# Performance work log

Measured on AMD Instinct MI355X. Metric: run time of the kernel, lower is better.

Reference implementation:

```python
import jax, jax.numpy as jnp
import numpy as np

H = 48; W = 48; C_IN = 32; C_OUT = 64
L = 4                      # liftsamples
RADIUS = 3                 # neighborhood radius
CMCO = 16                  # LieConv PointConv fixed mid channels
FOCAL = W / np.pi          # equidistant fisheye focal
CX, CY = (W - 1) / 2.0, (H - 1) / 2.0
EPS = 1e-7


def _build_neighbor_indices(h, w, radius):
    offs = [(dx, dy) for dy in range(-radius, radius + 1)
            for dx in range(-radius, radius + 1)
            if dx * dx + dy * dy <= radius * radius]
    offs = np.array(offs, dtype=np.int64)  # (k,2) as (dx,dy)
    yy, xx = np.meshgrid(np.arange(h), np.arange(w), indexing='ij')
    yy = yy.reshape(-1, 1); xx = xx.reshape(-1, 1)
    ny = yy + offs[None, :, 1]; nx = xx + offs[None, :, 0]
    valid = (ny >= 0) & (ny < h) & (nx >= 0) & (nx < w)
    idx = ny * w + nx
    return np.where(valid, idx, -1).astype(np.int32)  # (h*w, k)


def swish(x):
    return x * jax.nn.sigmoid(x)


def so3_exp(wvec):
    # Rodrigues: (...,3) -> (...,3,3)
    th = jnp.maximum(jnp.linalg.norm(wvec, axis=-1, keepdims=True), EPS)
    k = wvec / th
    kx, ky, kz = k[..., 0], k[..., 1], k[..., 2]
    z = jnp.zeros_like(kx)
    K = jnp.stack([jnp.stack([z, -kz, ky], -1),
                   jnp.stack([kz, z, -kx], -1),
                   jnp.stack([-ky, kx, z], -1)], -2)
    th = th[..., None]
    I = jnp.eye(3, dtype=wvec.dtype)
    return I + jnp.sin(th) * K + (1.0 - jnp.cos(th)) * (K @ K)


def so3_log(R):
    # (...,3,3) -> (...,3)
    tr = R[..., 0, 0] + R[..., 1, 1] + R[..., 2, 2]
    cos = jnp.clip((tr - 1.0) * 0.5, -1.0 + 1e-6, 1.0 - 1e-6)
    th = jnp.arccos(cos)
    v = jnp.stack([R[..., 2, 1] - R[..., 1, 2],
                   R[..., 0, 2] - R[..., 2, 0],
                   R[..., 1, 0] - R[..., 0, 1]], -1)
    return v * (th / (2.0 * jnp.sin(th)))[..., None]


def setup_inputs() -> dict:
    key = jax.random.key(0)
    ks = jax.random.split(key, 6)
    def lin(k, fi, fo):
        return jax.random.normal(k, (fi, fo), jnp.float32) / np.sqrt(fi)
    return {
        'x': jax.random.normal(ks[0], (2, C_IN, H, W), jnp.float32),
        'neighbor_idx': jnp.asarray(_build_neighbor_indices(H, W, RADIUS)),
        'W1': lin(ks[1], 3, 32), 'b1': jnp.zeros((32,), jnp.float32),
        'W2': lin(ks[2], 32, 32), 'b2': jnp.zeros((32,), jnp.float32),
        'W3': lin(ks[3], 32, CMCO), 'b3': jnp.zeros((CMCO,), jnp.float32),
        'Wl': lin(ks[4], CMCO * C_IN, C_OUT), 'bl': jnp.zeros((C_OUT,), jnp.float32),
    }


def _lift_log(dtype):
    # pixel grid -> unit rays -> so(3) log of lifted group elems, shape (n*L, 3)
    u = jnp.arange(W, dtype=dtype); v = jnp.arange(H, dtype=dtype)
    uu, vv = jnp.meshgrid(u, v)               # 'xy' indexing, (H,W)
    dx = (uu - CX).reshape(-1); dy = (vv - CY).reshape(-1)
    r = jnp.sqrt(dx * dx + dy * dy)
    theta = r / FOCAL
    rs = jnp.maximum(r, EPS)
    rays = jnp.stack([jnp.sin(theta) * dx / rs,
                      jnp.sin(theta) * dy / rs,
                      jnp.cos(theta)], -1)    # (n,3)
    pz = jnp.clip(rays[:, 2], -1.0 + 1e-6, 1.0 - 1e-6)
    ang = jnp.arccos(pz)
    axis = jnp.stack([-rays[:, 1], rays[:, 0], jnp.zeros_like(pz)], -1)
    axis = axis / jnp.maximum(jnp.linalg.norm(axis, axis=-1, keepdims=True), EPS)
    Rp = so3_exp(axis * ang[:, None])          # (n,3,3), Rp @ e3 = ray
    alphas = jnp.arange(L, dtype=dtype) * (2.0 * np.pi / L)
    Rz = so3_exp(jnp.stack([jnp.zeros_like(alphas), jnp.zeros_like(alphas), alphas], -1))
    Rlift = jnp.einsum('nij,ljk->nlik', Rp, Rz)  # (n,L,3,3)
    return so3_log(Rlift).reshape(H * W * L, 3)


def reference(x, neighbor_idx, W1, b1, W2, b2, W3, b3, Wl, bl):
    bs, c, h, w = x.shape
    n = h * w
    k = neighbor_idx.shape[1]
    nL, K = n * L, k * L

    a = _lift_log(x.dtype)                                   # (nL,3)

    valid = neighbor_idx >= 0                                # (n,k)
    safe_pix = jnp.maximum(neighbor_idx, 0).astype(jnp.int32)
    # lifted neighbor indices: query lift copy l sees all (j, l') neighbors
    nb_lift = safe_pix[:, None, :, None] * L + jnp.arange(L, dtype=jnp.int32)[None, None, None, :]
    nb_lift = jnp.broadcast_to(nb_lift, (n, L, k, L)).reshape(nL, K)
    nb_pix = jnp.broadcast_to(safe_pix[:, None, :, None], (n, L, k, L)).reshape(nL, K)
    mask = jnp.broadcast_to(valid[:, None, :, None], (n, L, k, L)).reshape(nL, K)

    # pairwise group elements: log(exp(-b) @ exp(a))
    b_log = a[nb_lift]                                       # (nL,K,3)
    Rab = jnp.einsum('qmij,qjk->qmik', so3_exp(-b_log), so3_exp(a))
    ab = so3_log(Rab)                                        # (nL,K,3)

    # kernel MLP (WeightNet: 3 -> 32 -> 32 -> 16, swish)
    hdn = swish(ab @ W1 + b1)
    hdn = swish(hdn @ W2 + b2)
    wts = swish(hdn @ W3 + b3)                               # (nL,K,16)
    wts = jnp.where(mask[..., None], wts, 0.0)

    values = x.transpose(0, 2, 3, 1).reshape(bs, n, c)       # (bs,n,c)
    nv = values[:, nb_pix]                                   # (bs,nL,K,c)
    partial = jnp.einsum('bqmc,qmf->bqcf', nv, wts).reshape(bs, nL, c * CMCO)
    out = partial @ Wl + bl                                  # (bs,nL,c_out)
    out = out.reshape(bs, n, L, -1).mean(axis=2)             # pool over lift samples
    return out.reshape(bs, h, w, -1).transpose(0, 3, 1, 2)   # (bs,c_out,h,w)
```

## Files before the change

kernel.cpp:

```cpp
#include <hip/hip_runtime.h>

#define WW   48
#define NPIX 2304
#define CIN  32
#define COUT 64
#define KNB  29
#define FCO  16
#define NPJ  (NPIX * KNB)

#define WS_RP64 0
#define WS_EG   165888
#define WS_M0   1050624
#define WS_V    1050688
#define WS_PART 4257856

__device__ __forceinline__ float swish_f(float x) {
    return x * __builtin_amdgcn_rcpf(1.0f + __expf(-x));
}

__device__ __forceinline__ void so3_exp_d(double wx, double wy, double wz, double R[9]) {
    double n  = sqrt(wx * wx + wy * wy + wz * wz);
    double th = fmax(n, 1e-7);
    double kx = wx / th, ky = wy / th, kz = wz / th;
    double s = sin(th), c = cos(th);
    double omc = 1.0 - c;
    R[0] = 1.0 + omc * (kx * kx - 1.0);
    R[1] = -s * kz + omc * kx * ky;
    R[2] =  s * ky + omc * kx * kz;
    R[3] =  s * kz + omc * kx * ky;
    R[4] = 1.0 + omc * (ky * ky - 1.0);
    R[5] = -s * kx + omc * ky * kz;
    R[6] = -s * ky + omc * kz * kx;
    R[7] =  s * kx + omc * kz * ky;
    R[8] = 1.0 + omc * (kz * kz - 1.0);
}

__device__ __forceinline__ void compute_Rp_d(int p, double R[9]) {
    int ui = p % WW, vi = p / WW;
    double dx = (double)ui - 23.5;
    double dy = (double)vi - 23.5;
    double r  = sqrt(dx * dx + dy * dy);
    const double FOCAL = 48.0 / 3.14159265358979323846;
    double theta = r / FOCAL;
    double rs = fmax(r, 1e-7);
    double st = sin(theta);
    double rayx = st * dx / rs;
    double rayy = st * dy / rs;
    double rayz = cos(theta);
    double pz  = fmin(fmax(rayz, -1.0 + 1e-6), 1.0 - 1e-6);
    double ang = acos(pz);
    double ax = -rayy, ay = rayx;
    double an = fmax(sqrt(ax * ax + ay * ay), 1e-7);
    ax /= an; ay /= an;
    so3_exp_d(ax * ang, ay * ang, 0.0, R);
}

__device__ __forceinline__ void mlp_half(float ab0, float ab1, float ab2, int Q0,
    const float* __restrict__ W1, const float* __restrict__ b1,
    const float* __restrict__ W2, const float* __restrict__ b2,
    const float* __restrict__ W3, const float* __restrict__ b3,
    float* acc3) {
    float accq[16];
    #pragma unroll
    for (int q = 0; q < 16; ++q) accq[q] = b2[Q0 + q];
    #pragma unroll
    for (int i = 0; i < 32; ++i) {
        float h = swish_f(b1[i] + ab0 * W1[i] + ab1 * W1[32 + i] + ab2 * W1[64 + i]);
        #pragma unroll
        for (int q = 0; q < 16; ++q) accq[q] += h * W2[i * 32 + Q0 + q];
    }
    #pragma unroll
    for (int q = 0; q < 16; ++q) {
        float h2 = swish_f(accq[q]);
        #pragma unroll
        for (int f = 0; f < FCO; ++f) acc3[f] += h2 * W3[(Q0 + q) * FCO + f];
    }
}

__device__ __forceinline__ void mlp_eval(float ab0, float ab1, float ab2,
    const float* __restrict__ W1, const float* __restrict__ b1,
    const float* __restrict__ W2, const float* __restrict__ b2,
    const float* __restrict__ W3, const float* __restrict__ b3,
    float* o) {
    float acc3[FCO];
    #pragma unroll
    for (int f = 0; f < FCO; ++f) acc3[f] = b3[f];
    mlp_half(ab0, ab1, ab2, 0,  W1, b1, W2, b2, W3, b3, acc3);
    __builtin_amdgcn_sched_barrier(0);
    mlp_half(ab0, ab1, ab2, 16, W1, b1, W2, b2, W3, b3, acc3);
    #pragma unroll
    for (int f = 0; f < FCO; ++f) o[f] = swish_f(acc3[f]);
}

__global__ __launch_bounds__(256)
void prep_kernel(const float* __restrict__ W1, const float* __restrict__ b1,
                 const float* __restrict__ W2, const float* __restrict__ b2,
                 const float* __restrict__ W3, const float* __restrict__ b3,
                 double* __restrict__ rp64, float* __restrict__ eg,
                 float* __restrict__ m0v) {
    int g = blockIdx.x * 256 + threadIdx.x;
    if (g > NPIX * 6) return;
    if (g == NPIX * 6) {
        float o[FCO];
        mlp_eval(0.f, 0.f, 0.f, W1, b1, W2, b2, W3, b3, o);
        #pragma unroll
        for (int f = 0; f < FCO; ++f) m0v[f] = o[f];
        return;
    }
    int pix = g / 6, which = g - pix * 6;
    double R[9];
    compute_Rp_d(pix, R);
    if (which == 0) {
        #pragma unroll
        for (int e = 0; e < 9; ++e) rp64[pix * 9 + e] = R[e];
    }
    int m = (which < 3) ? which : (which - 3);
    int l = m + (m >> 1);
    double c = (l == 0) ? 1.0 : 0.0;
    double s = (l == 1) ? 1.0 : ((l == 3) ? -1.0 : 0.0);
    double M[9];
    #pragma unroll
    for (int i = 0; i < 3; ++i) {
        M[i * 3 + 0] =  R[i * 3 + 0] * c + R[i * 3 + 1] * s;
        M[i * 3 + 1] = -R[i * 3 + 0] * s + R[i * 3 + 1] * c;
        M[i * 3 + 2] =  R[i * 3 + 2];
    }
    double tr   = M[0] + M[4] + M[8];
    double cosv = fmin(fmax((tr - 1.0) * 0.5, -1.0 + 1e-6), 1.0 - 1e-6);
    double th   = acos(cosv);
    double sv   = sqrt((1.0 - cosv) * (1.0 + cosv));
    double fac  = th / (2.0 * sv);
    float sg = (which < 3) ? 1.f : -1.f;
    float o[FCO];
    mlp_eval(sg * (float)((M[7] - M[5]) * fac),
             sg * (float)((M[2] - M[6]) * fac),
             sg * (float)((M[3] - M[1]) * fac),
             W1, b1, W2, b2, W3, b3, o);
    #pragma unroll
    for (int f = 0; f < FCO; ++f) eg[g * FCO + f] = o[f];
}

__global__ __launch_bounds__(256)
void vlog_kernel(const int* __restrict__ nbr, const double* __restrict__ rp64,
                 float* __restrict__ vws) {
    int tid = blockIdx.x * 256 + threadIdx.x;
    if (tid >= NPJ) return;
    int p = tid / KNB, j = tid - p * KNB;
    int idx = nbr[p * KNB + j];
    int pj = max(idx, 0);
    double Rq[9], Rn[9];
    #pragma unroll
    for (int e = 0; e < 9; ++e) Rq[e] = rp64[p * 9 + e];
    #pragma unroll
    for (int e = 0; e < 9; ++e) Rn[e] = rp64[pj * 9 + e];
    double X[9];
    #pragma unroll
    for (int i = 0; i < 3; ++i)
        #pragma unroll
        for (int jj = 0; jj < 3; ++jj) {
            double acc = 0.0;
            #pragma unroll
            for (int kk = 0; kk < 3; ++kk)
                acc += Rn[kk * 3 + i] * Rq[kk * 3 + jj];
            X[i * 3 + jj] = acc;
        }
    float* dst = vws + tid * 12;
    #pragma unroll
    for (int d = 0; d < 4; ++d) {
        double c = (d == 0) ? 1.0 : ((d == 2) ? -1.0 : 0.0);
        double s = (d == 1) ? 1.0 : ((d == 3) ? -1.0 : 0.0);
        double M0 =  X[0] * c + X[1] * s;
        double M1 = -X[0] * s + X[1] * c;
        double M2 =  X[2];
        double M3 =  X[3] * c + X[4] * s;
        double M4 = -X[3] * s + X[4] * c;
        double M5 =  X[5];
        double M6 =  X[6] * c + X[7] * s;
        double M7 = -X[6] * s + X[7] * c;
        double M8 =  X[8];
        double tr   = M0 + M4 + M8;
        double cosv = fmin(fmax((tr - 1.0) * 0.5, -1.0 + 1e-6), 1.0 - 1e-6);
        double th   = acos(cosv);
        double svv  = sqrt((1.0 - cosv) * (1.0 + cosv));
        double fac  = th / (2.0 * svv);
        dst[d * 3 + 0] = (float)((M7 - M5) * fac);
        dst[d * 3 + 1] = (float)((M2 - M6) * fac);
        dst[d * 3 + 2] = (float)((M3 - M1) * fac);
    }
}

__global__ __launch_bounds__(256)
void mlp1_kernel(const float* __restrict__ W1, const float* __restrict__ b1,
                 const float* __restrict__ W2, const float* __restrict__ b2,
                 const float* __restrict__ W3, const float* __restrict__ b3,
                 const float* __restrict__ vws, float* __restrict__ part) {
    int wave = blockIdx.x * 4 + (threadIdx.x >> 6);
    int lane = threadIdx.x & 63;
    int slot = lane / 9;
    int e    = lane - slot * 9;
    int g2   = wave * 7 + slot;
    int g2c  = min(g2, NPJ - 1);
    int l1m = e / 3, l2m = e - l1m * 3;
    int l1 = l1m + (l1m >> 1);
    int l2 = l2m + (l2m >> 1);
    int d  = (l1 - l2) & 3;
    const float* vp = vws + g2c * 12 + d * 3;
    float v0 = vp[0], v1 = vp[1], v2 = vp[2];
    float ab0 = (l2m == 0) ? v0 : ((l2m == 1) ?  v1 : -v1);
    float ab1 = (l2m == 0) ? v1 : ((l2m == 1) ? -v0 :  v0);
    float o[FCO];
    mlp_eval(ab0, ab1, v2, W1, b1, W2, b2, W3, b3, o);
    #pragma unroll
    for (int f = 0; f < FCO; ++f) {
        float a = o[f];
        a += __shfl(a, min(lane + 1, 63)) + __shfl(a, min(lane + 2, 63));
        a += __shfl(a, min(lane + 3, 63)) + __shfl(a, min(lane + 6, 63));
        o[f] = a;
    }
    if (e == 0 && lane < 63 && g2 < NPJ) {
        float* dst = part + g2 * FCO;
        #pragma unroll
        for (int f = 0; f < FCO; ++f) dst[f] = o[f];
    }
}

__global__ __launch_bounds__(256)
void agg_kernel(const float* __restrict__ x, const int* __restrict__ nbr,
                const float* __restrict__ Wl, const float* __restrict__ bl,
                const float* __restrict__ eg, const float* __restrict__ m0v,
                const float* __restrict__ part, float* __restrict__ out) {
    __shared__ int   spj[KNB];
    __shared__ int   sval[KNB];
    __shared__ float sE[FCO];
    __shared__ float sS[KNB][FCO];
    __shared__ float sxv[2][CIN][KNB];
    __shared__ float sT[2][CIN][FCO];
    __shared__ float spp[256];

    const int p = blockIdx.x;
    const int t = threadIdx.x;

    if (t < KNB) {
        int idx = nbr[p * KNB + t];
        spj[t]  = max(idx, 0);
        sval[t] = (idx >= 0) ? 1 : 0;
    } else if (t >= 32 && t < 32 + FCO) {
        int f = t - 32;
        sE[f] = eg[(p * 6 + 0) * FCO + f] + eg[(p * 6 + 1) * FCO + f]
              + eg[(p * 6 + 2) * FCO + f] + m0v[f];
    }
    __syncthreads();

    for (int e = t; e < 2 * CIN * KNB; e += 256) {
        int bb = e / (CIN * KNB);
        int r  = e - bb * (CIN * KNB);
        int c  = r / KNB;
        int j  = r - c * KNB;
        sxv[bb][c][j] = x[bb * (CIN * NPIX) + c * NPIX + spj[j]];
    }
    for (int idx = t; idx < KNB * FCO; idx += 256) {
        int j = idx >> 4, f = idx & 15;
        float acc = part[(p * KNB + j) * FCO + f];
        int n6 = spj[j] * 6;
        acc += eg[(n6 + 3) * FCO + f] + eg[(n6 + 4) * FCO + f] + eg[(n6 + 5) * FCO + f];
        acc += sE[f];
        sS[j][f] = sval[j] ? acc * 0.25f : 0.f;
    }
    __syncthreads();

    for (int tt = t; tt < 2 * CIN * FCO; tt += 256) {
        int bb = tt >> 9;
        int c  = (tt >> 4) & 31;
        int f  = tt & 15;
        float acc = 0.f;
        #pragma unroll
        for (int j = 0; j < KNB; ++j)
            acc += sxv[bb][c][j] * sS[j][f];
        sT[bb][c][f] = acc;
    }
    __syncthreads();

    {
        int half = t >> 7, q = t & 127, bb = q >> 6, co = q & 63;
        const float* Tb = &sT[bb][0][0];
        float acc = 0.f;
        int cf0 = half * 256;
        #pragma unroll 8
        for (int cf = cf0; cf < cf0 + 256; ++cf)
            acc += Tb[cf] * Wl[cf * COUT + co];
        spp[t] = acc;
    }
    __syncthreads();
    if (t < 128) {
        int bb = t >> 6, co = t & 63;
        out[bb * (COUT * NPIX) + co * NPIX + p] = spp[t] + spp[t + 128] + bl[co];
    }
}

extern "C" void kernel_launch(void* const* d_in, const int* in_sizes, int n_in,
                              void* d_out, int out_size, void* d_ws, size_t ws_size,
                              hipStream_t stream) {
    const float* x  = (const float*)d_in[0];
    const int* nbr  = (const int*)d_in[1];
    const float* W1 = (const float*)d_in[2];
    const float* b1 = (const float*)d_in[3];
    const float* W2 = (const float*)d_in[4];
    const float* b2 = (const float*)d_in[5];
    const float* W3 = (const float*)d_in[6];
    const float* b3 = (const float*)d_in[7];
    const float* Wl = (const float*)d_in[8];
    const float* bl = (const float*)d_in[9];
    float* out = (float*)d_out;

    char* ws = (char*)d_ws;
    double* rp64 = (double*)(ws + WS_RP64);
    float*  eg   = (float*)(ws + WS_EG);
    float*  m0v  = (float*)(ws + WS_M0);
    float*  vws  = (float*)(ws + WS_V);
    float*  part = (float*)(ws + WS_PART);

    hipLaunchKernelGGL(prep_kernel, dim3((NPIX * 6 + 1 + 255) / 256), dim3(256), 0, stream,
                       W1, b1, W2, b2, W3, b3, rp64, eg, m0v);
    hipLaunchKernelGGL(vlog_kernel, dim3((NPJ + 255) / 256), dim3(256), 0, stream,
                       nbr, rp64, vws);
    int waves = (NPJ + 6) / 7;
    int blocks = (waves + 3) / 4;
    hipLaunchKernelGGL(mlp1_kernel, dim3(blocks), dim3(256), 0, stream,
                       W1, b1, W2, b2, W3, b3, vws, part);
    hipLaunchKernelGGL(agg_kernel, dim3(NPIX), dim3(256), 0, stream,
                       x, nbr, Wl, bl, eg, m0v, part, out);
}
```

Before: 92.94 us.

## Fuse pairwise log computation into MLP kernel and merge edge-table work

Splits pixel rotation computation into a small rp_kernel, then fuses the pairwise relative-rotation log (formerly vlog_kernel) directly into the per-lane MLP evaluation, so the intermediate vws buffer is no longer written and reread. The per-pixel edge MLP table work (formerly in prep_kernel) is merged into the same launch as extra blocks, so the two independent workloads run concurrently and the launch count drops from four to three. Each lane now recomputes its own double-precision 3x3 product and acos for its direction instead of sharing a 4-direction result per pair, which adds redundant FP64 work in exchange for removing the memory round-trip and a launch.

```diff
diff --git a/kernel.cpp b/kernel.cpp
--- a/kernel.cpp
+++ b/kernel.cpp
@@ -7,12 +7,14 @@
 #define KNB  29
 #define FCO  16
 #define NPJ  (NPIX * KNB)
+#define GEN_WAVES  ((NPJ + 6) / 7)
+#define GEN_BLOCKS ((GEN_WAVES + 3) / 4)
+#define EDGE_BLOCKS ((NPIX * 6 + 1 + 255) / 256)
 
 #define WS_RP64 0
 #define WS_EG   165888
 #define WS_M0   1050624
-#define WS_V    1050688
-#define WS_PART 4257856
+#define WS_PART 1050688
 
 __device__ __forceinline__ float swish_f(float x) {
     return x * __builtin_amdgcn_rcpf(1.0f + __expf(-x));
@@ -55,7 +57,7 @@
     so3_exp_d(ax * ang, ay * ang, 0.0, R);
 }
 
-__device__ __forceinline__ void mlp_half(float ab0, float ab1, float ab2, int Q0,
+__device__ __forceinline__ void mlp_half(float ab0, float ab1, float ab2, const int Q0,
     const float* __restrict__ W1, const float* __restrict__ b1,
     const float* __restrict__ W2, const float* __restrict__ b2,
     const float* __restrict__ W3, const float* __restrict__ b3,
@@ -93,80 +95,54 @@
 }
 
 __global__ __launch_bounds__(256)
-void prep_kernel(const float* __restrict__ W1, const float* __restrict__ b1,
-                 const float* __restrict__ W2, const float* __restrict__ b2,
-                 const float* __restrict__ W3, const float* __restrict__ b3,
-                 double* __restrict__ rp64, float* __restrict__ eg,
-                 float* __restrict__ m0v) {
-    int g = blockIdx.x * 256 + threadIdx.x;
-    if (g > NPIX * 6) return;
-    if (g == NPIX * 6) {
-        float o[FCO];
-        mlp_eval(0.f, 0.f, 0.f, W1, b1, W2, b2, W3, b3, o);
-        #pragma unroll
-        for (int f = 0; f < FCO; ++f) m0v[f] = o[f];
-        return;
-    }
-    int pix = g / 6, which = g - pix * 6;
+void rp_kernel(double* __restrict__ rp64) {
+    int p = blockIdx.x * 256 + threadIdx.x;
+    if (p >= NPIX) return;
     double R[9];
-    compute_Rp_d(pix, R);
-    if (which == 0) {
-        #pragma unroll
-        for (int e = 0; e < 9; ++e) rp64[pix * 9 + e] = R[e];
-    }
-    int m = (which < 3) ? which : (which - 3);
-    int l = m + (m >> 1);
-    double c = (l == 0) ? 1.0 : 0.0;
-    double s = (l == 1) ? 1.0 : ((l == 3) ? -1.0 : 0.0);
-    double M[9];
-    #pragma unroll
-    for (int i = 0; i < 3; ++i) {
-        M[i * 3 + 0] =  R[i * 3 + 0] * c + R[i * 3 + 1] * s;
-        M[i * 3 + 1] = -R[i * 3 + 0] * s + R[i * 3 + 1] * c;
-        M[i * 3 + 2] =  R[i * 3 + 2];
-    }
-    double tr   = M[0] + M[4] + M[8];
-    double cosv = fmin(fmax((tr - 1.0) * 0.5, -1.0 + 1e-6), 1.0 - 1e-6);
-    double th   = acos(cosv);
-    double sv   = sqrt((1.0 - cosv) * (1.0 + cosv));
-    double fac  = th / (2.0 * sv);
-    float sg = (which < 3) ? 1.f : -1.f;
-    float o[FCO];
-    mlp_eval(sg * (float)((M[7] - M[5]) * fac),
-             sg * (float)((M[2] - M[6]) * fac),
-             sg * (float)((M[3] - M[1]) * fac),
-             W1, b1, W2, b2, W3, b3, o);
-    #pragma unroll
-    for (int f = 0; f < FCO; ++f) eg[g * FCO + f] = o[f];
+    compute_Rp_d(p, R);
+    #pragma unroll
+    for (int e = 0; e < 9; ++e) rp64[p * 9 + e] = R[e];
 }
 
 __global__ __launch_bounds__(256)
-void vlog_kernel(const int* __restrict__ nbr, const double* __restrict__ rp64,
-                 float* __restrict__ vws) {
-    int tid = blockIdx.x * 256 + threadIdx.x;
-    if (tid >= NPJ) return;
-    int p = tid / KNB, j = tid - p * KNB;
-    int idx = nbr[p * KNB + j];
-    int pj = max(idx, 0);
-    double Rq[9], Rn[9];
-    #pragma unroll
-    for (int e = 0; e < 9; ++e) Rq[e] = rp64[p * 9 + e];
-    #pragma unroll
-    for (int e = 0; e < 9; ++e) Rn[e] = rp64[pj * 9 + e];
-    double X[9];
-    #pragma unroll
-    for (int i = 0; i < 3; ++i)
-        #pragma unroll
-        for (int jj = 0; jj < 3; ++jj) {
-            double acc = 0.0;
+void fused_kernel(const int* __restrict__ nbr,
+                  const float* __restrict__ W1, const float* __restrict__ b1,
+                  const float* __restrict__ W2, const float* __restrict__ b2,
+                  const float* __restrict__ W3, const float* __restrict__ b3,
+                  const double* __restrict__ rp64,
+                  float* __restrict__ eg, float* __restrict__ m0v,
+                  float* __restrict__ part) {
+    if (blockIdx.x < GEN_BLOCKS) {
+        int wave = blockIdx.x * 4 + (threadIdx.x >> 6);
+        int lane = threadIdx.x & 63;
+        int slot = lane / 9;
+        int e    = lane - slot * 9;
+        int g2   = wave * 7 + slot;
+        int g2c  = min(g2, NPJ - 1);
+        int p = g2c / KNB, j = g2c - p * KNB;
+        int pj = max(nbr[p * KNB + j], 0);
+        int l1m = e / 3, l2m = e - l1m * 3;
+        int l1 = l1m + (l1m >> 1);
+        int l2 = l2m + (l2m >> 1);
+        int d  = (l1 - l2) & 3;
+        double Rq[9];
+        #pragma unroll
+        for (int q = 0; q < 9; ++q) Rq[q] = rp64[p * 9 + q];
+        double X[9];
+        #pragma unroll
+        for (int q = 0; q < 9; ++q) X[q] = 0.0;
+        #pragma unroll
+        for (int k = 0; k < 3; ++k) {
+            double rn0 = rp64[pj * 9 + k * 3 + 0];
+            double rn1 = rp64[pj * 9 + k * 3 + 1];
+            double rn2 = rp64[pj * 9 + k * 3 + 2];
             #pragma unroll
-            for (int kk = 0; kk < 3; ++kk)
-                acc += Rn[kk * 3 + i] * Rq[kk * 3 + jj];
-            X[i * 3 + jj] = acc;
-        }
-    float* dst = vws + tid * 12;
-    #pragma unroll
-    for (int d = 0; d < 4; ++d) {
+            for (int jj = 0; jj < 3; ++jj) {
+                X[0 * 3 + jj] += rn0 * Rq[k * 3 + jj];
+                X[1 * 3 + jj] += rn1 * Rq[k * 3 + jj];
+                X[2 * 3 + jj] += rn2 * Rq[k * 3 + jj];
+            }
+        }
         double c = (d == 0) ? 1.0 : ((d == 2) ? -1.0 : 0.0);
         double s = (d == 1) ? 1.0 : ((d == 3) ? -1.0 : 0.0);
         double M0 =  X[0] * c + X[1] * s;
@@ -183,44 +159,64 @@
         double th   = acos(cosv);
         double svv  = sqrt((1.0 - cosv) * (1.0 + cosv));
         double fac  = th / (2.0 * svv);
-        dst[d * 3 + 0] = (float)((M7 - M5) * fac);
-        dst[d * 3 + 1] = (float)((M2 - M6) * fac);
-        dst[d * 3 + 2] = (float)((M3 - M1) * fac);
-    }
-}
-
-__global__ __launch_bounds__(256)
-void mlp1_kernel(const float* __restrict__ W1, const float* __restrict__ b1,
-                 const float* __restrict__ W2, const float* __restrict__ b2,
-                 const float* __restrict__ W3, const float* __restrict__ b3,
-                 const float* __restrict__ vws, float* __restrict__ part) {
-    int wave = blockIdx.x * 4 + (threadIdx.x >> 6);
-    int lane = threadIdx.x & 63;
-    int slot = lane / 9;
-    int e    = lane - slot * 9;
-    int g2   = wave * 7 + slot;
-    int g2c  = min(g2, NPJ - 1);
-    int l1m = e / 3, l2m = e - l1m * 3;
-    int l1 = l1m + (l1m >> 1);
-    int l2 = l2m + (l2m >> 1);
-    int d  = (l1 - l2) & 3;
-    const float* vp = vws + g2c * 12 + d * 3;
-    float v0 = vp[0], v1 = vp[1], v2 = vp[2];
-    float ab0 = (l2m == 0) ? v0 : ((l2m == 1) ?  v1 : -v1);
-    float ab1 = (l2m == 0) ? v1 : ((l2m == 1) ? -v0 :  v0);
-    float o[FCO];
-    mlp_eval(ab0, ab1, v2, W1, b1, W2, b2, W3, b3, o);
-    #pragma unroll
-    for (int f = 0; f < FCO; ++f) {
-        float a = o[f];
-        a += __shfl(a, min(lane + 1, 63)) + __shfl(a, min(lane + 2, 63));
-        a += __shfl(a, min(lane + 3, 63)) + __shfl(a, min(lane + 6, 63));
-        o[f] = a;
-    }
-    if (e == 0 && lane < 63 && g2 < NPJ) {
-        float* dst = part + g2 * FCO;
-        #pragma unroll
-        for (int f = 0; f < FCO; ++f) dst[f] = o[f];
+        float v0 = (float)((M7 - M5) * fac);
+        float v1 = (float)((M2 - M6) * fac);
+        float v2 = (float)((M3 - M1) * fac);
+        float ab0 = (l2m == 0) ? v0 : ((l2m == 1) ?  v1 : -v1);
+        float ab1 = (l2m == 0) ? v1 : ((l2m == 1) ? -v0 :  v0);
+        __builtin_amdgcn_sched_barrier(0);
+        float o[FCO];
+        mlp_eval(ab0, ab1, v2, W1, b1, W2, b2, W3, b3, o);
+        #pragma unroll
+        for (int f = 0; f < FCO; ++f) {
+            float a = o[f];
+            a += __shfl(a, min(lane + 1, 63)) + __shfl(a, min(lane + 2, 63));
+            a += __shfl(a, min(lane + 3, 63)) + __shfl(a, min(lane + 6, 63));
+            o[f] = a;
+        }
+        if (e == 0 && lane < 63 && g2 < NPJ) {
+            float* dst = part + g2 * FCO;
+            #pragma unroll
+            for (int f = 0; f < FCO; ++f) dst[f] = o[f];
+        }
+    } else {
+        int g = (blockIdx.x - GEN_BLOCKS) * 256 + threadIdx.x;
+        if (g > NPIX * 6) return;
+        if (g == NPIX * 6) {
+            float o[FCO];
+            mlp_eval(0.f, 0.f, 0.f, W1, b1, W2, b2, W3, b3, o);
+            #pragma unroll
+            for (int f = 0; f < FCO; ++f) m0v[f] = o[f];
+            return;
+        }
+        int pix = g / 6, which = g - pix * 6;
+        double R[9];
+        #pragma unroll
+        for (int q = 0; q < 9; ++q) R[q] = rp64[pix * 9 + q];
+        int m = (which < 3) ? which : (which - 3);
+        int l = m + (m >> 1);
+        double c = (l == 0) ? 1.0 : 0.0;
+        double s = (l == 1) ? 1.0 : ((l == 3) ? -1.0 : 0.0);
+        double M[9];
+        #pragma unroll
+        for (int i = 0; i < 3; ++i) {
+            M[i * 3 + 0] =  R[i * 3 + 0] * c + R[i * 3 + 1] * s;
+            M[i * 3 + 1] = -R[i * 3 + 0] * s + R[i * 3 + 1] * c;
+            M[i * 3 + 2] =  R[i * 3 + 2];
+        }
+        double tr   = M[0] + M[4] + M[8];
+        double cosv = fmin(fmax((tr - 1.0) * 0.5, -1.0 + 1e-6), 1.0 - 1e-6);
+        double th   = acos(cosv);
+        double sv   = sqrt((1.0 - cosv) * (1.0 + cosv));
+        double fac  = th / (2.0 * sv);
+        float sg = (which < 3) ? 1.f : -1.f;
+        float o[FCO];
+        mlp_eval(sg * (float)((M[7] - M[5]) * fac),
+                 sg * (float)((M[2] - M[6]) * fac),
+                 sg * (float)((M[3] - M[1]) * fac),
+                 W1, b1, W2, b2, W3, b3, o);
+        #pragma unroll
+        for (int f = 0; f < FCO; ++f) eg[g * FCO + f] = o[f];
     }
 }
 
@@ -316,17 +312,12 @@
     double* rp64 = (double*)(ws + WS_RP64);
     float*  eg   = (float*)(ws + WS_EG);
     float*  m0v  = (float*)(ws + WS_M0);
-    float*  vws  = (float*)(ws + WS_V);
     float*  part = (float*)(ws + WS_PART);
 
-    hipLaunchKernelGGL(prep_kernel, dim3((NPIX * 6 + 1 + 255) / 256), dim3(256), 0, stream,
-                       W1, b1, W2, b2, W3, b3, rp64, eg, m0v);
-    hipLaunchKernelGGL(vlog_kernel, dim3((NPJ + 255) / 256), dim3(256), 0, stream,
-                       nbr, rp64, vws);
-    int waves = (NPJ + 6) / 7;
-    int blocks = (waves + 3) / 4;
-    hipLaunchKernelGGL(mlp1_kernel, dim3(blocks), dim3(256), 0, stream,
-                       W1, b1, W2, b2, W3, b3, vws, part);
+    hipLaunchKernelGGL(rp_kernel, dim3((NPIX + 255) / 256), dim3(256), 0, stream,
+                       rp64);
+    hipLaunchKernelGGL(fused_kernel, dim3(GEN_BLOCKS + EDGE_BLOCKS), dim3(256), 0, stream,
+                       nbr, W1, b1, W2, b2, W3, b3, rp64, eg, m0v, part);
     hipLaunchKernelGGL(agg_kernel, dim3(NPIX), dim3(256), 0, stream,
                        x, nbr, Wl, bl, eg, m0v, part, out);
 }
```

New measurement: 87.37 us, median of 2. 6.0% less time.
